# Performance work log

Measured on AMD Instinct MI355X. Metric: run time of the kernel, lower is better.

Reference implementation:

```python
import jax, jax.numpy as jnp
import numpy as np

B, S, SK = 4, 1024, 1024
Q_IN, KV_IN = 1024, 1024
G, DQ, DV = 16, 64, 64
OUT = Q_IN
EPS = 1e-5


def setup_inputs() -> dict:
    key = jax.random.key(0)
    ks = jax.random.split(key, 12)
    s_q = 1.0 / np.sqrt(Q_IN)
    s_kv = 1.0 / np.sqrt(KV_IN)
    s_p = 1.0 / np.sqrt(G * DV)
    return {
        "Q": jax.random.normal(ks[0], (B, S, Q_IN), jnp.float32),
        "KV": jax.random.normal(ks[1], (B, SK, KV_IN), jnp.float32),
        "Wq": jax.random.normal(ks[2], (G * DQ, Q_IN), jnp.float32) * s_q,
        "bq": jax.random.normal(ks[3], (G * DQ,), jnp.float32) * s_q,
        "Wk": jax.random.normal(ks[4], (G * DQ, KV_IN), jnp.float32) * s_kv,
        "bk": jax.random.normal(ks[5], (G * DQ,), jnp.float32) * s_kv,
        "Wv": jax.random.normal(ks[6], (G * DV, KV_IN), jnp.float32) * s_kv,
        "bv": jax.random.normal(ks[7], (G * DV,), jnp.float32) * s_kv,
        "Wp": jax.random.normal(ks[8], (OUT, G * DV), jnp.float32) * s_p,
        "bp": jax.random.normal(ks[9], (OUT,), jnp.float32) * s_p,
        "gamma": jnp.ones((OUT,), jnp.float32),
        "beta": jnp.zeros((OUT,), jnp.float32),
    }


def reference(Q, KV, Wq, bq, Wk, bk, Wv, bv, Wp, bp, gamma, beta):
    b, s, _ = Q.shape
    sk = KV.shape[1]
    inv_sqrt_dim = DQ ** (-0.5)

    # projections
    q = Q @ Wq.T + bq            # [b, s, G*DQ]
    k = KV @ Wk.T + bk           # [b, sk, G*DQ]
    v = KV @ Wv.T + bv           # [b, sk, G*DV]

    # q/k: group is the SLOW axis; v: group is the FAST axis (faithful to source)
    q = q.reshape(b, s, G, DQ)               # [b, s, g, d]
    k = k.reshape(b, sk, G, DQ)              # [b, sk, g, d]
    v = v.reshape(b, sk, DV, G)              # [b, sk, d, g]

    logits = jnp.einsum('bsgd,btgd->bgst', q, k) * inv_sqrt_dim  # [b, g, s, sk]
    scores = jax.nn.softmax(logits, axis=-1)
    attn = jnp.einsum('bgst,btdg->bgsd', scores, v)              # [b, g, s, dv]

    # flatten as (dv, g): feature index = d*G + g  (faithful to source permute)
    attn = attn.transpose(0, 2, 3, 1).reshape(b, s, DV * G)
    out = attn @ Wp.T + bp + Q

    # LayerNorm
    mu = out.mean(axis=-1, keepdims=True)
    var = out.var(axis=-1, keepdims=True)
    out = (out - mu) * jax.lax.rsqrt(var + EPS) * gamma + beta

    return out, scores.reshape(b * G, s, sk)
```

## Files before the change

kernel.cpp:

```cpp
#include <hip/hip_runtime.h>

typedef __attribute__((ext_vector_type(8))) short short8;
typedef __attribute__((ext_vector_type(4))) short s16x4;
typedef __attribute__((ext_vector_type(4))) float f32x4;

static __device__ __forceinline__ short f2bf(float x) {
  union { float f; unsigned u; } v; v.f = x;
  unsigned r = (v.u + 0x7fffu + ((v.u >> 16) & 1u)) >> 16;
  return (short)r;
}
static __device__ __forceinline__ float bf2f(short x) {
  union { unsigned u; float f; } v; v.u = ((unsigned)(unsigned short)x) << 16;
  return v.f;
}

static __device__ __forceinline__ void gld16(const short* g, short* l) {
  __builtin_amdgcn_global_load_lds(
      (const __attribute__((address_space(1))) unsigned*)g,
      (__attribute__((address_space(3))) unsigned*)l, 16, 0, 0);
}

__global__ __launch_bounds__(256) void convert_f32_bf16(const float* __restrict__ src,
                                                        short* __restrict__ dst, int n8,
                                                        float scale) {
  int i = blockIdx.x * 256 + threadIdx.x;
  if (i >= n8) return;
  const f32x4* s = (const f32x4*)(src + (long)i * 8);
  f32x4 a = s[0], b = s[1];
  short8 o;
  o[0] = f2bf(a[0] * scale); o[1] = f2bf(a[1] * scale);
  o[2] = f2bf(a[2] * scale); o[3] = f2bf(a[3] * scale);
  o[4] = f2bf(b[0] * scale); o[5] = f2bf(b[1] * scale);
  o[6] = f2bf(b[2] * scale); o[7] = f2bf(b[3] * scale);
  *(short8*)(dst + (long)i * 8) = o;
}

__global__ __launch_bounds__(256) void scale_bias(const float* __restrict__ src,
                                                  float* __restrict__ dst) {
  int i = blockIdx.x * 256 + threadIdx.x;
  dst[i] = src[i] * 0.125f;
}

__global__ __launch_bounds__(256) void convert_permute_wp(const float* __restrict__ src,
                                                          short* __restrict__ dst) {
  __shared__ float row[1024];
  const long o = blockIdx.x;
  *(f32x4*)&row[threadIdx.x * 4] = *(const f32x4*)(src + o * 1024 + threadIdx.x * 4);
  __syncthreads();
  const int f0 = threadIdx.x * 4;
  s16x4 t;
#pragma unroll
  for (int j = 0; j < 4; ++j) {
    int f = f0 + j;
    t[j] = f2bf(row[((f & 63) << 4) + (f >> 6)]);
  }
  *(s16x4*)(dst + o * 1024 + f0) = t;
}

template <int OMODE, typename OutT>
__global__ __launch_bounds__(256, 4) void gemm_mfma(
    const short* __restrict__ A, int lda,
    const short* __restrict__ B, int ldb,
    OutT* __restrict__ Cb, int ldc,
    const float* __restrict__ bias,
    const float* __restrict__ resid, int ldres,
    float scale, int K, int nbn) {
  __shared__ short As[64 * 64];
  __shared__ short Bs[64 * 64];

  const int nwg = gridDim.x, cpx = nwg >> 3;
  int bid = blockIdx.x;
  bid = (bid & 7) * cpx + (bid >> 3);
  const int bn = (bid % nbn) * 64, bm = (bid / nbn) * 64;

  const int tid = threadIdx.x, lane = tid & 63, wave = tid >> 6;
  const int fr = lane & 15, khi = lane >> 4;

  f32x4 acc[4];
#pragma unroll
  for (int n = 0; n < 4; ++n) acc[n] = (f32x4){0.f, 0.f, 0.f, 0.f};

  for (int k0 = 0; k0 < K; k0 += 64) {
#pragma unroll
    for (int it = 0; it < 2; ++it) {
      int l = it * 256 + tid;
      int r = l >> 3, c = (l & 7) ^ (r & 7);
      gld16(A + (long)(bm + r) * lda + k0 + c * 8, &As[l * 8]);
      gld16(B + (long)(bn + r) * ldb + k0 + c * 8, &Bs[l * 8]);
    }
    __syncthreads();
#pragma unroll
    for (int ks = 0; ks < 64; ks += 32) {
      const int cc = (ks >> 3) + khi;
      const int ar = wave * 16 + fr;
      short8 af = *(const short8*)&As[ar * 64 + (cc ^ (ar & 7)) * 8];
#pragma unroll
      for (int n = 0; n < 4; ++n) {
        const int br = n * 16 + fr;
        short8 bf = *(const short8*)&Bs[br * 64 + (cc ^ (br & 7)) * 8];
        acc[n] = __builtin_amdgcn_mfma_f32_16x16x32_bf16(af, bf, acc[n], 0, 0, 0);
      }
    }
    __syncthreads();
  }

  const int col0 = lane & 15, row0 = (lane >> 4) * 4;
#pragma unroll
  for (int n = 0; n < 4; ++n) {
    int gcol = bn + n * 16 + col0;
    float bi = bias ? bias[gcol] : 0.f;
#pragma unroll
    for (int i = 0; i < 4; ++i) {
      int grow = bm + wave * 16 + row0 + i;
      float v = acc[n][i] * scale + bi;
      if (resid) v += resid[(long)grow * ldres + gcol];
      long addr;
      if (OMODE == 0)
        addr = (long)grow * ldc + gcol;
      else
        addr = ((long)(grow >> 10) << 20) + ((long)gcol << 10) + (grow & 1023);
      if constexpr (sizeof(OutT) == 2)
        Cb[addr] = (OutT)f2bf(v);
      else
        Cb[addr] = v;
    }
  }
}

__global__ __launch_bounds__(512, 6) void fused_attn(
    const short* __restrict__ qb,
    const short* __restrict__ kb,
    const short* __restrict__ vt,
    float* __restrict__ scores,
    short* __restrict__ at) {
  constexpr int LP = 72;
  __shared__ short Ks[64 * 64];
  __shared__ short Vs[64 * 64];
  __shared__ short Ps[128 * LP];

  int bid = blockIdx.x;
  bid = (bid & 7) * 64 + (bid >> 3);
  const int z = bid >> 3, b = z >> 4, g = z & 15;
  const int q0 = (bid & 7) * 128;

  const int tid = threadIdx.x, lane = tid & 63, w = tid >> 6;
  const int fr = lane & 15, khi = lane >> 4;
  const long bqk = (long)b << 20;
  const int qr = q0 + w * 16;

  const short* qrow = qb + bqk + (long)(qr + fr) * 1024 + g * 64 + khi * 8;
  const short8 aq0 = *(const short8*)qrow;
  const short8 aq1 = *(const short8*)(qrow + 32);
  const short* kgp = kb + bqk + g * 64;
  const short* vgp = vt + bqk;

  const int srr = tid >> 3, ssc = ((tid & 7) ^ (srr & 7)) * 8;

  float s4[4] = {0.f, 0.f, 0.f, 0.f};
  for (int t0 = 0; t0 < 1024; t0 += 64) {
    gld16(kgp + (long)(t0 + srr) * 1024 + ssc, &Ks[tid * 8]);
    __syncthreads();
    f32x4 sacc[4];
#pragma unroll
    for (int nf = 0; nf < 4; ++nf) sacc[nf] = (f32x4){0.f, 0.f, 0.f, 0.f};
#pragma unroll
    for (int nf = 0; nf < 4; ++nf) {
      const int r2 = nf * 16 + fr;
      short8 b0 = *(const short8*)&Ks[r2 * 64 + (khi ^ (r2 & 7)) * 8];
      short8 b1 = *(const short8*)&Ks[r2 * 64 + ((khi + 4) ^ (r2 & 7)) * 8];
      sacc[nf] = __builtin_amdgcn_mfma_f32_16x16x32_bf16(aq0, b0, sacc[nf], 0, 0, 0);
      sacc[nf] = __builtin_amdgcn_mfma_f32_16x16x32_bf16(aq1, b1, sacc[nf], 0, 0, 0);
    }
#pragma unroll
    for (int nf = 0; nf < 4; ++nf)
#pragma unroll
      for (int i = 0; i < 4; ++i) s4[i] += __expf(sacc[nf][i]);
    __syncthreads();
  }
#pragma unroll
  for (int i = 0; i < 4; ++i) {
    s4[i] += __shfl_xor(s4[i], 1);
    s4[i] += __shfl_xor(s4[i], 2);
    s4[i] += __shfl_xor(s4[i], 4);
    s4[i] += __shfl_xor(s4[i], 8);
  }
  float inv4[4];
#pragma unroll
  for (int i = 0; i < 4; ++i) inv4[i] = 1.f / s4[i];

  f32x4 pacc[4];
#pragma unroll
  for (int nv = 0; nv < 4; ++nv) pacc[nv] = (f32x4){0.f, 0.f, 0.f, 0.f};

  for (int t0 = 0; t0 < 1024; t0 += 64) {
    gld16(kgp + (long)(t0 + srr) * 1024 + ssc, &Ks[tid * 8]);
    gld16(vgp + ((long)(srr * 16 + g) << 10) + t0 + ssc, &Vs[tid * 8]);
    __syncthreads();
    f32x4 sacc[4];
#pragma unroll
    for (int nf = 0; nf < 4; ++nf) sacc[nf] = (f32x4){0.f, 0.f, 0.f, 0.f};
#pragma unroll
    for (int nf = 0; nf < 4; ++nf) {
      const int r2 = nf * 16 + fr;
      short8 b0 = *(const short8*)&Ks[r2 * 64 + (khi ^ (r2 & 7)) * 8];
      short8 b1 = *(const short8*)&Ks[r2 * 64 + ((khi + 4) ^ (r2 & 7)) * 8];
      sacc[nf] = __builtin_amdgcn_mfma_f32_16x16x32_bf16(aq0, b0, sacc[nf], 0, 0, 0);
      sacc[nf] = __builtin_amdgcn_mfma_f32_16x16x32_bf16(aq1, b1, sacc[nf], 0, 0, 0);
    }
#pragma unroll
    for (int nf = 0; nf < 4; ++nf)
#pragma unroll
      for (int i = 0; i < 4; ++i)
        Ps[(w * 16 + khi * 4 + i) * LP + nf * 16 + fr] =
            f2bf(__expf(sacc[nf][i]) * inv4[i]);

#pragma unroll
    for (int ks = 0; ks < 64; ks += 32) {
      const int cc = (ks >> 3) + khi;
      short8 ap = *(const short8*)&Ps[(w * 16 + fr) * LP + ks + khi * 8];
#pragma unroll
      for (int nv = 0; nv < 4; ++nv) {
        const int dr = nv * 16 + fr;
        short8 bvv = *(const short8*)&Vs[dr * 64 + (cc ^ (dr & 7)) * 8];
        pacc[nv] = __builtin_amdgcn_mfma_f32_16x16x32_bf16(ap, bvv, pacc[nv], 0, 0, 0);
      }
    }

#pragma unroll
    for (int ri = 0; ri < 4; ++ri) {
      const int row = ri * 4 + khi;
      s16x4 pv4 = *(const s16x4*)&Ps[(w * 16 + row) * LP + fr * 4];
      f32x4 o;
      o[0] = bf2f(pv4[0]); o[1] = bf2f(pv4[1]);
      o[2] = bf2f(pv4[2]); o[3] = bf2f(pv4[3]);
      *(f32x4*)&scores[((long)z << 20) + ((long)(qr + row) << 10) + t0 + fr * 4] = o;
    }
    __syncthreads();
  }

#pragma unroll
  for (int nv = 0; nv < 4; ++nv)
#pragma unroll
    for (int i = 0; i < 4; ++i)
      at[bqk + ((long)(qr + khi * 4 + i) << 10) + g * 64 + nv * 16 + fr] =
          f2bf(pacc[nv][i]);
}

__global__ __launch_bounds__(256) void layernorm_rows(const float* __restrict__ X,
                                                      const float* __restrict__ gamma,
                                                      const float* __restrict__ beta,
                                                      float* __restrict__ O) {
  const int row = blockIdx.x * 4 + (threadIdx.x >> 6);
  const int lane = threadIdx.x & 63;
  const float* x = X + (long)row * 1024 + lane * 4;
  f32x4 v[4];
  float s = 0.f, sq = 0.f;
#pragma unroll
  for (int j = 0; j < 4; ++j) {
    v[j] = *(const f32x4*)(x + j * 256);
#pragma unroll
    for (int e = 0; e < 4; ++e) {
      s += v[j][e];
      sq += v[j][e] * v[j][e];
    }
  }
#pragma unroll
  for (int off = 32; off; off >>= 1) {
    s += __shfl_xor(s, off);
    sq += __shfl_xor(sq, off);
  }
  const float mu = s * (1.f / 1024.f);
  const float var = sq * (1.f / 1024.f) - mu * mu;
  const float rstd = rsqrtf(var + 1e-5f);
  float* o = O + (long)row * 1024 + lane * 4;
#pragma unroll
  for (int j = 0; j < 4; ++j) {
    f32x4 g = *(const f32x4*)(gamma + lane * 4 + j * 256);
    f32x4 be = *(const f32x4*)(beta + lane * 4 + j * 256);
    f32x4 r;
#pragma unroll
    for (int e = 0; e < 4; ++e) r[e] = (v[j][e] - mu) * rstd * g[e] + be[e];
    *(f32x4*)(o + j * 256) = r;
  }
}

extern "C" void kernel_launch(void* const* d_in, const int* in_sizes, int n_in,
                              void* d_out, int out_size, void* d_ws, size_t ws_size,
                              hipStream_t stream) {
  const float* Q = (const float*)d_in[0];
  const float* KV = (const float*)d_in[1];
  const float* Wq = (const float*)d_in[2];
  const float* bq = (const float*)d_in[3];
  const float* Wk = (const float*)d_in[4];
  const float* bk = (const float*)d_in[5];
  const float* Wv = (const float*)d_in[6];
  const float* bv = (const float*)d_in[7];
  const float* Wp = (const float*)d_in[8];
  const float* bp = (const float*)d_in[9];
  const float* gamma = (const float*)d_in[10];
  const float* beta = (const float*)d_in[11];

  float* out = (float*)d_out;
  float* scores = out + (long)4 * 1024 * 1024;

  char* ws = (char*)d_ws;
  short* Wqb = (short*)(ws);
  short* Wkb = (short*)(ws + (2L << 20));
  short* Wvb = (short*)(ws + (4L << 20));
  short* Wpb = (short*)(ws + (6L << 20));
  short* qb  = (short*)(ws + (8L << 20));
  short* kb  = (short*)(ws + (16L << 20));
  short* vt  = (short*)(ws + (24L << 20));
  short* at  = (short*)(ws + (32L << 20));
  float* pre = (float*)(ws + (40L << 20));
  short* Qb  = (short*)(ws + (40L << 20));
  short* KVb = (short*)(ws + (48L << 20));
  float* bqs = (float*)(ws + (56L << 20));
  (void)ws_size; (void)in_sizes; (void)n_in; (void)out_size;

  convert_f32_bf16<<<2048, 256, 0, stream>>>(Q, Qb, 524288, 1.f);
  convert_f32_bf16<<<2048, 256, 0, stream>>>(KV, KVb, 524288, 1.f);
  convert_f32_bf16<<<512, 256, 0, stream>>>(Wq, Wqb, 131072, 0.125f);
  convert_f32_bf16<<<512, 256, 0, stream>>>(Wk, Wkb, 131072, 1.f);
  convert_f32_bf16<<<512, 256, 0, stream>>>(Wv, Wvb, 131072, 1.f);
  convert_permute_wp<<<1024, 256, 0, stream>>>(Wp, Wpb);
  scale_bias<<<4, 256, 0, stream>>>(bq, bqs);

  gemm_mfma<0, short><<<1024, 256, 0, stream>>>(
      Qb, 1024, Wqb, 1024, qb, 1024, bqs, nullptr, 0, 1.f, 1024, 16);
  gemm_mfma<0, short><<<1024, 256, 0, stream>>>(
      KVb, 1024, Wkb, 1024, kb, 1024, bk, nullptr, 0, 1.f, 1024, 16);
  gemm_mfma<1, short><<<1024, 256, 0, stream>>>(
      KVb, 1024, Wvb, 1024, vt, 1024, bv, nullptr, 0, 1.f, 1024, 16);

  fused_attn<<<512, 512, 0, stream>>>(qb, kb, vt, scores, at);

  gemm_mfma<0, float><<<1024, 256, 0, stream>>>(
      at, 1024, Wpb, 1024, pre, 1024, bp, Q, 1024, 1.f, 1024, 16);

  layernorm_rows<<<1024, 256, 0, stream>>>(pre, gamma, beta, out);
}
```

Measured before the change: 198.5 us.

## Double-buffer LDS tiles in GEMM and fused attention to prefetch next tile

```diff
diff --git a/kernel.cpp b/kernel.cpp
--- a/kernel.cpp
+++ b/kernel.cpp
@@ -65,8 +65,8 @@
     const float* __restrict__ bias,
     const float* __restrict__ resid, int ldres,
     float scale, int K, int nbn) {
-  __shared__ short As[64 * 64];
-  __shared__ short Bs[64 * 64];
+  __shared__ short As[2][64 * 64];
+  __shared__ short Bs[2][64 * 64];
 
   const int nwg = gridDim.x, cpx = nwg >> 3;
   int bid = blockIdx.x;
@@ -80,28 +80,35 @@
 #pragma unroll
   for (int n = 0; n < 4; ++n) acc[n] = (f32x4){0.f, 0.f, 0.f, 0.f};
 
-  for (int k0 = 0; k0 < K; k0 += 64) {
+  auto stage = [&](int buf, int k0) {
 #pragma unroll
     for (int it = 0; it < 2; ++it) {
       int l = it * 256 + tid;
       int r = l >> 3, c = (l & 7) ^ (r & 7);
-      gld16(A + (long)(bm + r) * lda + k0 + c * 8, &As[l * 8]);
-      gld16(B + (long)(bn + r) * ldb + k0 + c * 8, &Bs[l * 8]);
-    }
-    __syncthreads();
+      gld16(A + (long)(bm + r) * lda + k0 + c * 8, &As[buf][l * 8]);
+      gld16(B + (long)(bn + r) * ldb + k0 + c * 8, &Bs[buf][l * 8]);
+    }
+  };
+
+  stage(0, 0);
+  __syncthreads();
+  int cur = 0;
+  for (int k0 = 0; k0 < K; k0 += 64) {
+    if (k0 + 64 < K) stage(cur ^ 1, k0 + 64);
 #pragma unroll
     for (int ks = 0; ks < 64; ks += 32) {
       const int cc = (ks >> 3) + khi;
       const int ar = wave * 16 + fr;
-      short8 af = *(const short8*)&As[ar * 64 + (cc ^ (ar & 7)) * 8];
+      short8 af = *(const short8*)&As[cur][ar * 64 + (cc ^ (ar & 7)) * 8];
 #pragma unroll
       for (int n = 0; n < 4; ++n) {
         const int br = n * 16 + fr;
-        short8 bf = *(const short8*)&Bs[br * 64 + (cc ^ (br & 7)) * 8];
+        short8 bf = *(const short8*)&Bs[cur][br * 64 + (cc ^ (br & 7)) * 8];
         acc[n] = __builtin_amdgcn_mfma_f32_16x16x32_bf16(af, bf, acc[n], 0, 0, 0);
       }
     }
     __syncthreads();
+    cur ^= 1;
   }
 
   const int col0 = lane & 15, row0 = (lane >> 4) * 4;
@@ -134,8 +141,8 @@
     float* __restrict__ scores,
     short* __restrict__ at) {
   constexpr int LP = 72;
-  __shared__ short Ks[64 * 64];
-  __shared__ short Vs[64 * 64];
+  __shared__ short Ks[2][64 * 64];
+  __shared__ short Vs[2][64 * 64];
   __shared__ short Ps[128 * LP];
 
   int bid = blockIdx.x;
@@ -157,17 +164,20 @@
   const int srr = tid >> 3, ssc = ((tid & 7) ^ (srr & 7)) * 8;
 
   float s4[4] = {0.f, 0.f, 0.f, 0.f};
+  gld16(kgp + (long)srr * 1024 + ssc, &Ks[0][tid * 8]);
+  __syncthreads();
+  int cur = 0;
   for (int t0 = 0; t0 < 1024; t0 += 64) {
-    gld16(kgp + (long)(t0 + srr) * 1024 + ssc, &Ks[tid * 8]);
-    __syncthreads();
+    if (t0 < 960)
+      gld16(kgp + (long)(t0 + 64 + srr) * 1024 + ssc, &Ks[cur ^ 1][tid * 8]);
     f32x4 sacc[4];
 #pragma unroll
     for (int nf = 0; nf < 4; ++nf) sacc[nf] = (f32x4){0.f, 0.f, 0.f, 0.f};
 #pragma unroll
     for (int nf = 0; nf < 4; ++nf) {
       const int r2 = nf * 16 + fr;
-      short8 b0 = *(const short8*)&Ks[r2 * 64 + (khi ^ (r2 & 7)) * 8];
-      short8 b1 = *(const short8*)&Ks[r2 * 64 + ((khi + 4) ^ (r2 & 7)) * 8];
+      short8 b0 = *(const short8*)&Ks[cur][r2 * 64 + (khi ^ (r2 & 7)) * 8];
+      short8 b1 = *(const short8*)&Ks[cur][r2 * 64 + ((khi + 4) ^ (r2 & 7)) * 8];
       sacc[nf] = __builtin_amdgcn_mfma_f32_16x16x32_bf16(aq0, b0, sacc[nf], 0, 0, 0);
       sacc[nf] = __builtin_amdgcn_mfma_f32_16x16x32_bf16(aq1, b1, sacc[nf], 0, 0, 0);
     }
@@ -176,6 +186,7 @@
 #pragma unroll
       for (int i = 0; i < 4; ++i) s4[i] += __expf(sacc[nf][i]);
     __syncthreads();
+    cur ^= 1;
   }
 #pragma unroll
   for (int i = 0; i < 4; ++i) {
@@ -192,18 +203,23 @@
 #pragma unroll
   for (int nv = 0; nv < 4; ++nv) pacc[nv] = (f32x4){0.f, 0.f, 0.f, 0.f};
 
+  gld16(kgp + (long)srr * 1024 + ssc, &Ks[0][tid * 8]);
+  gld16(vgp + ((long)(srr * 16 + g) << 10) + ssc, &Vs[0][tid * 8]);
+  __syncthreads();
+  cur = 0;
   for (int t0 = 0; t0 < 1024; t0 += 64) {
-    gld16(kgp + (long)(t0 + srr) * 1024 + ssc, &Ks[tid * 8]);
-    gld16(vgp + ((long)(srr * 16 + g) << 10) + t0 + ssc, &Vs[tid * 8]);
-    __syncthreads();
+    if (t0 < 960) {
+      gld16(kgp + (long)(t0 + 64 + srr) * 1024 + ssc, &Ks[cur ^ 1][tid * 8]);
+      gld16(vgp + ((long)(srr * 16 + g) << 10) + t0 + 64 + ssc, &Vs[cur ^ 1][tid * 8]);
+    }
     f32x4 sacc[4];
 #pragma unroll
     for (int nf = 0; nf < 4; ++nf) sacc[nf] = (f32x4){0.f, 0.f, 0.f, 0.f};
 #pragma unroll
     for (int nf = 0; nf < 4; ++nf) {
       const int r2 = nf * 16 + fr;
-      short8 b0 = *(const short8*)&Ks[r2 * 64 + (khi ^ (r2 & 7)) * 8];
-      short8 b1 = *(const short8*)&Ks[r2 * 64 + ((khi + 4) ^ (r2 & 7)) * 8];
+      short8 b0 = *(const short8*)&Ks[cur][r2 * 64 + (khi ^ (r2 & 7)) * 8];
+      short8 b1 = *(const short8*)&Ks[cur][r2 * 64 + ((khi + 4) ^ (r2 & 7)) * 8];
       sacc[nf] = __builtin_amdgcn_mfma_f32_16x16x32_bf16(aq0, b0, sacc[nf], 0, 0, 0);
       sacc[nf] = __builtin_amdgcn_mfma_f32_16x16x32_bf16(aq1, b1, sacc[nf], 0, 0, 0);
     }
@@ -221,7 +237,7 @@
 #pragma unroll
       for (int nv = 0; nv < 4; ++nv) {
         const int dr = nv * 16 + fr;
-        short8 bvv = *(const short8*)&Vs[dr * 64 + (cc ^ (dr & 7)) * 8];
+        short8 bvv = *(const short8*)&Vs[cur][dr * 64 + (cc ^ (dr & 7)) * 8];
         pacc[nv] = __builtin_amdgcn_mfma_f32_16x16x32_bf16(ap, bvv, pacc[nv], 0, 0, 0);
       }
     }
@@ -236,6 +252,7 @@
       *(f32x4*)&scores[((long)z << 20) + ((long)(qr + row) << 10) + t0 + fr * 4] = o;
     }
     __syncthreads();
+    cur ^= 1;
   }
 
 #pragma unroll
```

New measurement: 193.1 us. 1.03x faster.
